# Performance work log

Measured on AMD Instinct MI355X. Metric: run time of the kernel, lower is better.

Reference implementation:

```python
import jax, jax.numpy as jnp
import numpy as np

B = 2_097_152
EPS = 1e-6


def setup_inputs() -> dict:
    key = jax.random.key(0)
    k0, k1, k2, k3, k4, k5, k6 = jax.random.split(key, 7)
    out0 = jax.random.normal(k0, (B, 1), dtype=jnp.float32)
    # softmax head is consumed as probabilities (torch.log(pred) directly)
    out1 = jax.random.uniform(k1, (B, 8), dtype=jnp.float32, minval=EPS, maxval=1.0 - EPS)
    out2 = jax.random.normal(k2, (B, 4), dtype=jnp.float32)
    out3 = jax.random.normal(k3, (B, 1), dtype=jnp.float32)
    out4 = jax.random.normal(k4, (B, 1), dtype=jnp.float32)
    targets = jax.random.randint(k5, (B, 15), 0, 2).astype(jnp.int32)
    pos_dist = jax.random.uniform(k6, (15,), dtype=jnp.float32, minval=0.05, maxval=0.95)
    return {"out0": out0, "out1": out1, "out2": out2, "out3": out3,
            "out4": out4, "pos_dist": pos_dist, "targets": targets}


def _sig(x):
    return jnp.clip(jax.nn.sigmoid(x), EPS, 1.0 - EPS)


def _clc_loss_mask(pred, gt, pos_weight):
    # pred, gt: [B] floats, gt in {0,1}
    pos = gt == 1.0
    neg = gt == 0.0
    pos_loss = jnp.sum(jnp.where(pos, jnp.log(pred) * jnp.square(1.0 - pred) * pos_weight, 0.0))
    neg_loss = jnp.sum(jnp.where(neg, jnp.log(1.0 - pred) * jnp.square(pred) * (1.0 - pos_weight), 0.0))
    n = (jnp.sum(pos) + jnp.sum(neg)).astype(pred.dtype)
    return -jnp.where(n > 0, (pos_loss + neg_loss) / jnp.maximum(n, 1.0), 0.0)


def _binary_head(out, gt_col, pw):
    p = _sig(out)[:, 0]
    loss = _clc_loss_mask(p, gt_col, pw)
    succ = jnp.sum((p > 0.5).astype(jnp.int32) == gt_col.astype(jnp.int32))
    return loss, succ


def _softmax_head(out, gt_blk, w):
    # out: [B,C] probabilities, gt_blk: [B,C] one-hot-ish, w: [C]
    mask = gt_blk == 1.0
    num = jnp.sum(mask).astype(out.dtype)
    pos_loss = jnp.sum(jnp.where(mask, jnp.log(out) * jnp.square(1.0 - out) * w[None, :], 0.0))
    loss = -jnp.where(num > 0, pos_loss / jnp.maximum(num, 1.0), 0.0)
    succ = jnp.sum(jnp.argmax(gt_blk, axis=1) == jnp.argmax(out, axis=1))
    return loss, succ


def _bce_head(out, gt_blk, w):
    # out: [B,C] logits; per-element weight = 1-w[j] where gt==1 else w[j]
    weights = jnp.where(gt_blk == 1.0, 1.0 - w[None, :], w[None, :])
    bce = jnp.clip(out, 0.0, None) - out * gt_blk + jnp.log1p(jnp.exp(-jnp.abs(out)))
    loss = jnp.mean(weights * bce)
    succ = jnp.sum((out > 0.5).astype(jnp.int32) == gt_blk.astype(jnp.int32))
    return loss, succ


def reference(out0, out1, out2, out3, out4, pos_dist, targets):
    t = targets.astype(jnp.float32)
    # column layout (class_value=[1,8,4,1,1]):
    # idx0 -> col 0 ; idx1 -> cols 1:9 ; idx2 -> cols 9:13 ; idx3 -> col 13 ; idx4 -> col 14
    l0, s0 = _binary_head(out0, t[:, 0], 1.0 - pos_dist[0])
    l1, s1 = _softmax_head(out1, t[:, 1:9], 1.0 - pos_dist[1:9])
    l2, s2 = _bce_head(out2, t[:, 9:13], pos_dist[9:13])
    l3, s3 = _binary_head(out3, t[:, 13], 1.0 - pos_dist[13])
    l4, s4 = _binary_head(out4, t[:, 14], 1.0 - pos_dist[14])
    loss = l0 + l1 + l2 + l3 + l4
    label_number = 1 + 1 + 4 + 1 + 1  # binary heads count 1, bce head counts its width
    pred_success = (s0 + s1 + s2 + s3 + s4).astype(jnp.float32)
    acc = pred_success / label_number
    return loss.reshape(1), acc
```

## Files before the change

### kernel.cpp

```cpp
#include <hip/hip_runtime.h>
#include <math.h>

#define BROWS 2097152
#define NTH 256
#define NBLOCKS (BROWS / NTH)
#define FINAL_NTH 1024

constexpr float FEPS = 1e-6f;

__device__ __forceinline__ float wave_reduce_f(float v) {
#pragma unroll
    for (int off = 32; off > 0; off >>= 1) v += __shfl_down(v, off, 64);
    return v;
}

__device__ __forceinline__ double wave_reduce_d(double v) {
#pragma unroll
    for (int off = 32; off > 0; off >>= 1) v += __shfl_down(v, off, 64);
    return v;
}

__global__ __launch_bounds__(256) void loss_main(
    const float* __restrict__ out0, const float* __restrict__ out1,
    const float* __restrict__ out2, const float* __restrict__ out3,
    const float* __restrict__ out4, const float* __restrict__ pos_dist,
    const int* __restrict__ targets, float* __restrict__ partials)
{
    __shared__ int tl[4][15 * 64];
    __shared__ float sred[4][7];

    float pd[15];
#pragma unroll
    for (int j = 0; j < 15; ++j) pd[j] = pos_dist[j];

    const int tid = threadIdx.x;
    const int lane = tid & 63;
    const int wave = tid >> 6;
    const int row = blockIdx.x * NTH + tid;
    const int wrow0 = blockIdx.x * NTH + wave * 64;

    const long tb = (long)wrow0 * 15;
#pragma unroll
    for (int k = 0; k < 15; ++k)
        tl[wave][k * 64 + lane] = targets[tb + k * 64 + lane];

    const float x0 = out0[row];
    const float x3 = out3[row];
    const float x4 = out4[row];
    const float4 q2 = ((const float4*)out2)[row];
    const float4 pa = ((const float4*)out1)[(long)row * 2 + 0];
    const float4 pb = ((const float4*)out1)[(long)row * 2 + 1];

    int t[15];
#pragma unroll
    for (int j = 0; j < 15; ++j) t[j] = tl[wave][lane * 15 + j];

    float acc0, acc1 = 0.f, acc2 = 0.f, acc3, acc4;
    float cnt5 = 0.f, succ = 0.f;

    {
        float p = __builtin_amdgcn_rcpf(1.f + __expf(-x0));
        p = fminf(fmaxf(p, FEPS), 1.f - FEPS);
        float om = 1.f - p;
        bool pos = t[0] != 0;
        float larg = pos ? p : om;
        float quad = pos ? om : p;
        float coef = pos ? (1.f - pd[0]) : pd[0];
        acc0 = __logf(larg) * quad * quad * coef;
        succ += ((x0 > 0.f) == pos) ? 1.f : 0.f;
    }
    {
        float p = __builtin_amdgcn_rcpf(1.f + __expf(-x3));
        p = fminf(fmaxf(p, FEPS), 1.f - FEPS);
        float om = 1.f - p;
        bool pos = t[13] != 0;
        float larg = pos ? p : om;
        float quad = pos ? om : p;
        float coef = pos ? (1.f - pd[13]) : pd[13];
        acc3 = __logf(larg) * quad * quad * coef;
        succ += ((x3 > 0.f) == pos) ? 1.f : 0.f;
    }
    {
        float p = __builtin_amdgcn_rcpf(1.f + __expf(-x4));
        p = fminf(fmaxf(p, FEPS), 1.f - FEPS);
        float om = 1.f - p;
        bool pos = t[14] != 0;
        float larg = pos ? p : om;
        float quad = pos ? om : p;
        float coef = pos ? (1.f - pd[14]) : pd[14];
        acc4 = __logf(larg) * quad * quad * coef;
        succ += ((x4 > 0.f) == pos) ? 1.f : 0.f;
    }

    {
        const float o[8] = {pa.x, pa.y, pa.z, pa.w, pb.x, pb.y, pb.z, pb.w};
        int am_gt = 0;
#pragma unroll
        for (int j = 7; j >= 0; --j)
            if (t[1 + j] != 0) am_gt = j;
        float best = o[0];
        int am_o = 0;
#pragma unroll
        for (int j = 1; j < 8; ++j)
            if (o[j] > best) { best = o[j]; am_o = j; }
#pragma unroll
        for (int j = 0; j < 8; ++j) {
            float m = (t[1 + j] != 0) ? 1.f : 0.f;
            float om = 1.f - o[j];
            acc1 += m * (__logf(o[j]) * om * om * (1.f - pd[1 + j]));
            cnt5 += m;
        }
        succ += (am_gt == am_o) ? 1.f : 0.f;
    }

    {
        const float o2v[4] = {q2.x, q2.y, q2.z, q2.w};
#pragma unroll
        for (int j = 0; j < 4; ++j) {
            float o = o2v[j];
            bool g = t[9 + j] != 0;
            float w = pd[9 + j];
            float weight = g ? (1.f - w) : w;
            float bce = fmaxf(o, 0.f) - (g ? o : 0.f)
                      + __logf(1.f + __expf(-fabsf(o)));
            acc2 += weight * bce;
            succ += ((o > 0.5f) == g) ? 1.f : 0.f;
        }
    }

    {
        float accv[7] = {acc0, acc1, acc2, acc3, acc4, cnt5, succ};
#pragma unroll
        for (int k = 0; k < 7; ++k) {
            float v = wave_reduce_f(accv[k]);
            if (lane == 0) sred[wave][k] = v;
        }
    }
    __syncthreads();
    if (tid == 0) {
#pragma unroll
        for (int k = 0; k < 7; ++k) {
            float s = sred[0][k] + sred[1][k] + sred[2][k] + sred[3][k];
            partials[(long)blockIdx.x * 8 + k] = s;
        }
    }
}

__global__ __launch_bounds__(FINAL_NTH) void loss_final(
    const float* __restrict__ partials, int nblocks, float* __restrict__ out)
{
    double acc[7] = {0, 0, 0, 0, 0, 0, 0};
    for (int b = threadIdx.x; b < nblocks; b += FINAL_NTH) {
        const float4* pp = (const float4*)(partials + (long)b * 8);
        float4 a = pp[0], bb = pp[1];
        acc[0] += a.x; acc[1] += a.y; acc[2] += a.z; acc[3] += a.w;
        acc[4] += bb.x; acc[5] += bb.y; acc[6] += bb.z;
    }

    __shared__ double sd[16][7];
    const int lane = threadIdx.x & 63;
    const int wave = threadIdx.x >> 6;
#pragma unroll
    for (int k = 0; k < 7; ++k) {
        double v = wave_reduce_d(acc[k]);
        if (lane == 0) sd[wave][k] = v;
    }
    __syncthreads();
    if (threadIdx.x == 0) {
        double s[7];
#pragma unroll
        for (int k = 0; k < 7; ++k) {
            double t = 0.0;
#pragma unroll
            for (int w = 0; w < 16; ++w) t += sd[w][k];
            s[k] = t;
        }

        const double Bd = (double)BROWS;
        double l0 = -(s[0] / Bd);
        double num = s[5];
        double l1 = (num > 0.0) ? -(s[1] / fmax(num, 1.0)) : 0.0;
        double l2 = s[2] / (Bd * 4.0);
        double l3 = -(s[3] / Bd);
        double l4 = -(s[4] / Bd);
        out[0] = (float)(l0 + l1 + l2 + l3 + l4);
        out[1] = (float)(s[6] / 8.0);
    }
}

extern "C" void kernel_launch(void* const* d_in, const int* in_sizes, int n_in,
                              void* d_out, int out_size, void* d_ws, size_t ws_size,
                              hipStream_t stream) {
    const float* out0 = (const float*)d_in[0];
    const float* out1 = (const float*)d_in[1];
    const float* out2 = (const float*)d_in[2];
    const float* out3 = (const float*)d_in[3];
    const float* out4 = (const float*)d_in[4];
    const float* pos_dist = (const float*)d_in[5];
    const int* targets = (const int*)d_in[6];
    float* out = (float*)d_out;
    float* partials = (float*)d_ws;

    loss_main<<<NBLOCKS, NTH, 0, stream>>>(
        out0, out1, out2, out3, out4, pos_dist, targets, partials);
    loss_final<<<1, FINAL_NTH, 0, stream>>>(partials, NBLOCKS, out);
}
```

Baseline: 56.91 us.

## Process four row chunks per block and count successes with wave ballots

Each block now loops over four 256-row chunks, accumulating per-thread sums across chunks. This cuts the block count and partial-sum writes by four and shrinks the final reduction kernel to 256 threads. Integer success and mask counts are computed with ballot and popcount per wave instead of per-thread float sums reduced with shuffles. The trade-off is less parallelism per launch. The per-wave LDS staging buffer is also reused across chunks without a barrier, which relies on wave-level lockstep ordering.

After: 52.08 us. 8.5% less time.

```diff
diff --git a/kernel.cpp b/kernel.cpp
--- a/kernel.cpp
+++ b/kernel.cpp
@@ -3,8 +3,9 @@
 
 #define BROWS 2097152
 #define NTH 256
-#define NBLOCKS (BROWS / NTH)
-#define FINAL_NTH 1024
+#define CHUNKS_PER_BLOCK 4
+#define NBLOCKS (BROWS / (NTH * CHUNKS_PER_BLOCK))
+#define FINAL_NTH 256
 
 constexpr float FEPS = 1e-6f;
 
@@ -27,7 +28,7 @@
     const int* __restrict__ targets, float* __restrict__ partials)
 {
     __shared__ int tl[4][15 * 64];
-    __shared__ float sred[4][7];
+    __shared__ float sred[4][5];
 
     float pd[15];
 #pragma unroll
@@ -36,113 +37,128 @@
     const int tid = threadIdx.x;
     const int lane = tid & 63;
     const int wave = tid >> 6;
-    const int row = blockIdx.x * NTH + tid;
-    const int wrow0 = blockIdx.x * NTH + wave * 64;
-
-    const long tb = (long)wrow0 * 15;
-#pragma unroll
-    for (int k = 0; k < 15; ++k)
-        tl[wave][k * 64 + lane] = targets[tb + k * 64 + lane];
-
-    const float x0 = out0[row];
-    const float x3 = out3[row];
-    const float x4 = out4[row];
-    const float4 q2 = ((const float4*)out2)[row];
-    const float4 pa = ((const float4*)out1)[(long)row * 2 + 0];
-    const float4 pb = ((const float4*)out1)[(long)row * 2 + 1];
-
-    int t[15];
-#pragma unroll
-    for (int j = 0; j < 15; ++j) t[j] = tl[wave][lane * 15 + j];
-
-    float acc0, acc1 = 0.f, acc2 = 0.f, acc3, acc4;
-    float cnt5 = 0.f, succ = 0.f;
+
+    float acc0 = 0.f, acc1 = 0.f, acc2 = 0.f, acc3 = 0.f, acc4 = 0.f;
+    long long succ_i = 0, cnt5_i = 0;
+
+#pragma unroll
+    for (int c = 0; c < CHUNKS_PER_BLOCK; ++c) {
+        const int chunk = blockIdx.x * CHUNKS_PER_BLOCK + c;
+        const int row = chunk * NTH + tid;
+        const int wrow0 = chunk * NTH + wave * 64;
+
+        const long tb = (long)wrow0 * 15;
+#pragma unroll
+        for (int k = 0; k < 15; ++k)
+            tl[wave][k * 64 + lane] = targets[tb + k * 64 + lane];
+
+        const float x0 = out0[row];
+        const float x3 = out3[row];
+        const float x4 = out4[row];
+        const float4 q2 = ((const float4*)out2)[row];
+        const float4 pa = ((const float4*)out1)[(long)row * 2 + 0];
+        const float4 pb = ((const float4*)out1)[(long)row * 2 + 1];
+
+        int t[15];
+#pragma unroll
+        for (int j = 0; j < 15; ++j) t[j] = tl[wave][lane * 15 + j];
+
+        {
+            float p = __builtin_amdgcn_rcpf(1.f + __expf(-x0));
+            p = fminf(fmaxf(p, FEPS), 1.f - FEPS);
+            float om = 1.f - p;
+            bool pos = t[0] != 0;
+            float larg = pos ? p : om;
+            float quad = pos ? om : p;
+            float coef = pos ? (1.f - pd[0]) : pd[0];
+            acc0 += __logf(larg) * quad * quad * coef;
+            succ_i += __popcll(__ballot((x0 > 0.f) == pos));
+        }
+        {
+            float p = __builtin_amdgcn_rcpf(1.f + __expf(-x3));
+            p = fminf(fmaxf(p, FEPS), 1.f - FEPS);
+            float om = 1.f - p;
+            bool pos = t[13] != 0;
+            float larg = pos ? p : om;
+            float quad = pos ? om : p;
+            float coef = pos ? (1.f - pd[13]) : pd[13];
+            acc3 += __logf(larg) * quad * quad * coef;
+            succ_i += __popcll(__ballot((x3 > 0.f) == pos));
+        }
+        {
+            float p = __builtin_amdgcn_rcpf(1.f + __expf(-x4));
+            p = fminf(fmaxf(p, FEPS), 1.f - FEPS);
+            float om = 1.f - p;
+            bool pos = t[14] != 0;
+            float larg = pos ? p : om;
+            float quad = pos ? om : p;
+            float coef = pos ? (1.f - pd[14]) : pd[14];
+            acc4 += __logf(larg) * quad * quad * coef;
+            succ_i += __popcll(__ballot((x4 > 0.f) == pos));
+        }
+
+        {
+            const float o[8] = {pa.x, pa.y, pa.z, pa.w, pb.x, pb.y, pb.z, pb.w};
+            int am_gt = 0;
+#pragma unroll
+            for (int j = 7; j >= 0; --j)
+                if (t[1 + j] != 0) am_gt = j;
+            float best = o[0];
+            int am_o = 0;
+#pragma unroll
+            for (int j = 1; j < 8; ++j)
+                if (o[j] > best) { best = o[j]; am_o = j; }
+#pragma unroll
+            for (int j = 0; j < 8; ++j) {
+                bool m = t[1 + j] != 0;
+                float wsel = m ? (1.f - pd[1 + j]) : 0.f;
+                float om = 1.f - o[j];
+                acc1 += wsel * (__logf(o[j]) * om * om);
+                cnt5_i += __popcll(__ballot(m));
+            }
+            succ_i += __popcll(__ballot(am_gt == am_o));
+        }
+
+        {
+            const float o2v[4] = {q2.x, q2.y, q2.z, q2.w};
+#pragma unroll
+            for (int j = 0; j < 4; ++j) {
+                float o = o2v[j];
+                bool g = t[9 + j] != 0;
+                float w = pd[9 + j];
+                float weight = g ? (1.f - w) : w;
+                float bce = fmaxf(o, 0.f) - (g ? o : 0.f)
+                          + __logf(1.f + __expf(-fabsf(o)));
+                acc2 += weight * bce;
+                succ_i += __popcll(__ballot((o > 0.5f) == g));
+            }
+        }
+    }
 
     {
-        float p = __builtin_amdgcn_rcpf(1.f + __expf(-x0));
-        p = fminf(fmaxf(p, FEPS), 1.f - FEPS);
-        float om = 1.f - p;
-        bool pos = t[0] != 0;
-        float larg = pos ? p : om;
-        float quad = pos ? om : p;
-        float coef = pos ? (1.f - pd[0]) : pd[0];
-        acc0 = __logf(larg) * quad * quad * coef;
-        succ += ((x0 > 0.f) == pos) ? 1.f : 0.f;
-    }
-    {
-        float p = __builtin_amdgcn_rcpf(1.f + __expf(-x3));
-        p = fminf(fmaxf(p, FEPS), 1.f - FEPS);
-        float om = 1.f - p;
-        bool pos = t[13] != 0;
-        float larg = pos ? p : om;
-        float quad = pos ? om : p;
-        float coef = pos ? (1.f - pd[13]) : pd[13];
-        acc3 = __logf(larg) * quad * quad * coef;
-        succ += ((x3 > 0.f) == pos) ? 1.f : 0.f;
-    }
-    {
-        float p = __builtin_amdgcn_rcpf(1.f + __expf(-x4));
-        p = fminf(fmaxf(p, FEPS), 1.f - FEPS);
-        float om = 1.f - p;
-        bool pos = t[14] != 0;
-        float larg = pos ? p : om;
-        float quad = pos ? om : p;
-        float coef = pos ? (1.f - pd[14]) : pd[14];
-        acc4 = __logf(larg) * quad * quad * coef;
-        succ += ((x4 > 0.f) == pos) ? 1.f : 0.f;
-    }
-
-    {
-        const float o[8] = {pa.x, pa.y, pa.z, pa.w, pb.x, pb.y, pb.z, pb.w};
-        int am_gt = 0;
-#pragma unroll
-        for (int j = 7; j >= 0; --j)
-            if (t[1 + j] != 0) am_gt = j;
-        float best = o[0];
-        int am_o = 0;
-#pragma unroll
-        for (int j = 1; j < 8; ++j)
-            if (o[j] > best) { best = o[j]; am_o = j; }
-#pragma unroll
-        for (int j = 0; j < 8; ++j) {
-            float m = (t[1 + j] != 0) ? 1.f : 0.f;
-            float om = 1.f - o[j];
-            acc1 += m * (__logf(o[j]) * om * om * (1.f - pd[1 + j]));
-            cnt5 += m;
-        }
-        succ += (am_gt == am_o) ? 1.f : 0.f;
-    }
-
-    {
-        const float o2v[4] = {q2.x, q2.y, q2.z, q2.w};
-#pragma unroll
-        for (int j = 0; j < 4; ++j) {
-            float o = o2v[j];
-            bool g = t[9 + j] != 0;
-            float w = pd[9 + j];
-            float weight = g ? (1.f - w) : w;
-            float bce = fmaxf(o, 0.f) - (g ? o : 0.f)
-                      + __logf(1.f + __expf(-fabsf(o)));
-            acc2 += weight * bce;
-            succ += ((o > 0.5f) == g) ? 1.f : 0.f;
-        }
-    }
-
-    {
-        float accv[7] = {acc0, acc1, acc2, acc3, acc4, cnt5, succ};
-#pragma unroll
-        for (int k = 0; k < 7; ++k) {
+        float accv[5] = {acc0, acc1, acc2, acc3, acc4};
+#pragma unroll
+        for (int k = 0; k < 5; ++k) {
             float v = wave_reduce_f(accv[k]);
             if (lane == 0) sred[wave][k] = v;
         }
     }
+    __shared__ float scnt[4][2];
+    if (lane == 0) {
+        scnt[wave][0] = (float)cnt5_i;
+        scnt[wave][1] = (float)succ_i;
+    }
     __syncthreads();
     if (tid == 0) {
 #pragma unroll
-        for (int k = 0; k < 7; ++k) {
+        for (int k = 0; k < 5; ++k) {
             float s = sred[0][k] + sred[1][k] + sred[2][k] + sred[3][k];
             partials[(long)blockIdx.x * 8 + k] = s;
         }
+        partials[(long)blockIdx.x * 8 + 5] =
+            scnt[0][0] + scnt[1][0] + scnt[2][0] + scnt[3][0];
+        partials[(long)blockIdx.x * 8 + 6] =
+            scnt[0][1] + scnt[1][1] + scnt[2][1] + scnt[3][1];
     }
 }
 
@@ -157,7 +173,7 @@
         acc[4] += bb.x; acc[5] += bb.y; acc[6] += bb.z;
     }
 
-    __shared__ double sd[16][7];
+    __shared__ double sd[4][7];
     const int lane = threadIdx.x & 63;
     const int wave = threadIdx.x >> 6;
 #pragma unroll
@@ -169,12 +185,7 @@
     if (threadIdx.x == 0) {
         double s[7];
 #pragma unroll
-        for (int k = 0; k < 7; ++k) {
-            double t = 0.0;
-#pragma unroll
-            for (int w = 0; w < 16; ++w) t += sd[w][k];
-            s[k] = t;
-        }
+        for (int k = 0; k < 7; ++k) s[k] = sd[0][k] + sd[1][k] + sd[2][k] + sd[3][k];
 
         const double Bd = (double)BROWS;
         double l0 = -(s[0] / Bd);
```
